# Performance work log

Hardware: AMD Instinct MI355X
Metric: run time of the kernel (lower is better)

## Reference

```python
import jax, jax.numpy as jnp
import numpy as np

N_NODES = 100000
N_EDGES = 3200000
F_IN, F_HID, F_OUT = 128, 16, 32


def setup_inputs() -> dict:
    key = jax.random.key(0)
    k1, k2, k3, k4, k5, k6 = jax.random.split(key, 6)
    x = jax.random.normal(k1, (N_NODES, F_IN), dtype=jnp.float32)
    edge_index = jax.random.randint(k2, (2, N_EDGES), 0, N_NODES, dtype=jnp.int64)
    # Glorot-style init for GCNConv weights, zero bias (PyG defaults)
    W1 = jax.random.normal(k3, (F_IN, F_HID), dtype=jnp.float32) * (1.0 / np.sqrt(F_IN))
    b1 = jnp.zeros((F_HID,), dtype=jnp.float32)
    W2 = jax.random.normal(k4, (F_HID, F_OUT), dtype=jnp.float32) * (1.0 / np.sqrt(F_HID))
    b2 = jnp.zeros((F_OUT,), dtype=jnp.float32)
    return {"x": x, "edge_index": edge_index, "W1": W1, "b1": b1, "W2": W2, "b2": b2}


def reference(x, edge_index, W1, b1, W2, b2):
    N = x.shape[0]
    self_loops = jnp.arange(N, dtype=edge_index.dtype)
    row = jnp.concatenate([edge_index[0], self_loops])  # source nodes
    col = jnp.concatenate([edge_index[1], self_loops])  # target nodes
    # symmetric normalization: deg computed on targets (with self-loops)
    deg = jax.ops.segment_sum(jnp.ones_like(col, dtype=x.dtype), col, num_segments=N)
    dinv = jnp.where(deg > 0, jax.lax.rsqrt(deg), 0.0)
    norm = dinv[row] * dinv[col]  # [E+N]

    def gcn_conv(h, W, b):
        h = h @ W                                   # [N, out]
        msg = h[row] * norm[:, None]                # gather + scale [E+N, out]
        agg = jax.ops.segment_sum(msg, col, num_segments=N)  # scatter-add
        return agg + b

    h = jax.nn.relu(gcn_conv(x, W1, b1))
    # dropout is identity in eval mode
    out = gcn_conv(h, W2, b2)
    return jax.nn.log_softmax(out, axis=1)
```

## Files before the change

### kernel.cpp

```cpp
#include <hip/hip_runtime.h>
#include <math.h>

#define F_IN  128
#define F_HID 16
#define F_OUT 32
#define G     784
#define CSH   9
#define CN    512
#define MAXB  256
#define SCH   4096

typedef unsigned int u32;

__device__ inline float bflo(u32 d) { return __uint_as_float(d << 16); }
__device__ inline float bfhi(u32 d) { return __uint_as_float(d & 0xFFFF0000u); }
__device__ inline u32 f2bf(float f) {
    u32 u = __float_as_uint(f);
    return (u + 0x7FFFu + ((u >> 16) & 1u)) >> 16;
}
__device__ inline u32 pk2(float lo, float hi) { return f2bf(lo) | (f2bf(hi) << 16); }

__global__ void k_hist(const int* __restrict__ col, int E,
                       int* __restrict__ hist_t, int B) {
    __shared__ int h[MAXB];
    int t = threadIdx.x, g = blockIdx.x;
    for (int k = t; k < B; k += 256) h[k] = 0;
    __syncthreads();
    int cg = (E + G - 1) / G;
    int e0 = g * cg, e1 = min(E, e0 + cg);
    for (int e = e0 + t; e < e1; e += 256)
        atomicAdd(&h[col[e] >> CSH], 1);
    __syncthreads();
    for (int b = t; b < B; b += 256) hist_t[(size_t)b * G + g] = h[b];
}

__global__ void k_scan_part(const int* __restrict__ hist_t, int* __restrict__ psum,
                            int M) {
    __shared__ int sd[256];
    int t = threadIdx.x;
    int base = blockIdx.x * SCH + t * 16;
    int s = 0;
#pragma unroll
    for (int k = 0; k < 16; ++k) { int i = base + k; if (i < M) s += hist_t[i]; }
    sd[t] = s;
    __syncthreads();
    for (int o = 128; o > 0; o >>= 1) { if (t < o) sd[t] += sd[t + o]; __syncthreads(); }
    if (t == 0) psum[blockIdx.x] = sd[0];
}

__global__ void k_scan_top(int* __restrict__ psum, int NP) {
    __shared__ int sd[256];
    int t = threadIdx.x;
    int v = (t < NP) ? psum[t] : 0;
    sd[t] = v;
    __syncthreads();
    for (int o = 1; o < 256; o <<= 1) {
        int x = (t >= o) ? sd[t - o] : 0;
        __syncthreads();
        sd[t] += x;
        __syncthreads();
    }
    if (t < NP) psum[t] = sd[t] - v;
}

__global__ void k_scan_out(const int* __restrict__ hist_t, const int* __restrict__ psum,
                           int* __restrict__ off, int M) {
    __shared__ int sd[256];
    int t = threadIdx.x;
    int base = blockIdx.x * SCH + t * 16;
    int v[16], s = 0;
#pragma unroll
    for (int k = 0; k < 16; ++k) {
        v[k] = (base + k < M) ? hist_t[base + k] : 0;
        s += v[k];
    }
    sd[t] = s;
    __syncthreads();
    for (int o = 1; o < 256; o <<= 1) {
        int x = (t >= o) ? sd[t - o] : 0;
        __syncthreads();
        sd[t] += x;
        __syncthreads();
    }
    int run = psum[blockIdx.x] + sd[t] - s;
#pragma unroll
    for (int k = 0; k < 16; ++k) {
        int i = base + k;
        if (i < M) off[i] = run;
        run += v[k];
        if (i == M - 1) off[M] = run;
    }
}

__global__ void k_fill(const int* __restrict__ row, const int* __restrict__ col,
                       int E, const int* __restrict__ off, u32* __restrict__ pairs,
                       int B) {
    __shared__ int cur[MAXB];
    int t = threadIdx.x, g = blockIdx.x;
    for (int b = t; b < B; b += 256) cur[b] = off[(size_t)b * G + g];
    __syncthreads();
    int cg = (E + G - 1) / G;
    int e0 = g * cg, e1 = min(E, e0 + cg);
    for (int e = e0 + t; e < e1; e += 256) {
        int c = col[e];
        int p = atomicAdd(&cur[c >> CSH], 1);
        pairs[p] = ((u32)(c & (CN - 1)) << 17) | (u32)row[e];
    }
}

__global__ void __launch_bounds__(512)
k_sortfine(const u32* __restrict__ pairs, const int* __restrict__ off, int B, int E,
           int* __restrict__ nptr, float* __restrict__ dinv,
           int* __restrict__ srcs, int N) {
    __shared__ int cnt[CN];
    __shared__ int pre[CN];
    int t = threadIdx.x, b = blockIdx.x;
    cnt[t] = 0;
    __syncthreads();
    int s0 = off[(size_t)b * G];
    int s1 = (b == B - 1) ? E : off[(size_t)(b + 1) * G];
    for (int e = s0 + t; e < s1; e += 512)
        atomicAdd(&cnt[pairs[e] >> 17], 1);
    __syncthreads();
    int v = cnt[t];
    pre[t] = v;
    __syncthreads();
    for (int o = 1; o < 512; o <<= 1) {
        int x = (t >= o) ? pre[t - o] : 0;
        __syncthreads();
        pre[t] += x;
        __syncthreads();
    }
    int excl = pre[t] - v;
    int n = (b << CSH) + t;
    nptr[n] = s0 + excl;
    if (b == B - 1 && t == CN - 1) nptr[n + 1] = E;
    if (n < N) dinv[n] = rsqrtf((float)v + 1.0f);
    __syncthreads();
    cnt[t] = s0 + excl;
    __syncthreads();
    for (int e = s0 + t; e < s1; e += 512) {
        u32 p = pairs[e];
        int r = atomicAdd(&cnt[p >> 17], 1);
        srcs[r] = (int)(p & 0x1FFFFu);
    }
}

__global__ void k_gemm1(const float* __restrict__ x, const float* __restrict__ W1,
                        const float* __restrict__ dinv, u32* __restrict__ hs1b, int N) {
    __shared__ float sW[F_IN * F_HID];
    __shared__ float sX[16][F_IN + 4];
    int t = threadIdx.x;
    {
        const float4* W4 = (const float4*)W1;
        float4* sW4 = (float4*)sW;
#pragma unroll
        for (int k = t; k < F_IN * F_HID / 4; k += 256) sW4[k] = W4[k];
    }
    int node0 = blockIdx.x * 16;
    {
        const float4* x4 = (const float4*)(x + (size_t)node0 * F_IN);
#pragma unroll
        for (int k = t; k < 16 * F_IN / 4; k += 256) {
            int r = k >> 5, c4 = k & 31;
            float4 vv = (node0 + r < N) ? x4[k] : make_float4(0.f, 0.f, 0.f, 0.f);
            *(float4*)&sX[r][c4 * 4] = vv;
        }
    }
    __syncthreads();
    int il = t >> 4, j = t & 15;
    float acc = 0.f;
    const float* xr = sX[il];
#pragma unroll 8
    for (int k = 0; k < F_IN; ++k) acc += xr[k] * sW[k * F_HID + j];
    int n = node0 + il;
    float v = (n < N) ? acc * dinv[n] : 0.f;
    float other = __shfl_xor(v, 1);
    if (n < N && !(j & 1)) hs1b[(size_t)n * 8 + (j >> 1)] = pk2(v, other);
}

__device__ inline void gather16(const u32* __restrict__ src, const int* __restrict__ srcs,
                                int e0, int e1, int l, float* a) {
    const uint4* H = (const uint4*)src;
    int e = e0 + l;
    for (; e + 4 < e1; e += 8) {
        int i0 = srcs[e], i1 = srcs[e + 4];
        uint4 d0 = H[(size_t)i0 * 2], d1 = H[(size_t)i0 * 2 + 1];
        uint4 d2 = H[(size_t)i1 * 2], d3 = H[(size_t)i1 * 2 + 1];
        a[0] += bflo(d0.x) + bflo(d2.x);  a[1] += bfhi(d0.x) + bfhi(d2.x);
        a[2] += bflo(d0.y) + bflo(d2.y);  a[3] += bfhi(d0.y) + bfhi(d2.y);
        a[4] += bflo(d0.z) + bflo(d2.z);  a[5] += bfhi(d0.z) + bfhi(d2.z);
        a[6] += bflo(d0.w) + bflo(d2.w);  a[7] += bfhi(d0.w) + bfhi(d2.w);
        a[8] += bflo(d1.x) + bflo(d3.x);  a[9] += bfhi(d1.x) + bfhi(d3.x);
        a[10]+= bflo(d1.y) + bflo(d3.y);  a[11]+= bfhi(d1.y) + bfhi(d3.y);
        a[12]+= bflo(d1.z) + bflo(d3.z);  a[13]+= bfhi(d1.z) + bfhi(d3.z);
        a[14]+= bflo(d1.w) + bflo(d3.w);  a[15]+= bfhi(d1.w) + bfhi(d3.w);
    }
    if (e < e1) {
        int i0 = srcs[e];
        uint4 d0 = H[(size_t)i0 * 2], d1 = H[(size_t)i0 * 2 + 1];
        a[0] += bflo(d0.x);  a[1] += bfhi(d0.x);
        a[2] += bflo(d0.y);  a[3] += bfhi(d0.y);
        a[4] += bflo(d0.z);  a[5] += bfhi(d0.z);
        a[6] += bflo(d0.w);  a[7] += bfhi(d0.w);
        a[8] += bflo(d1.x);  a[9] += bfhi(d1.x);
        a[10]+= bflo(d1.y);  a[11]+= bfhi(d1.y);
        a[12]+= bflo(d1.z);  a[13]+= bfhi(d1.z);
        a[14]+= bflo(d1.w);  a[15]+= bfhi(d1.w);
    }
}

__global__ void k_agg1(const u32* __restrict__ hs1b, const int* __restrict__ srcs,
                       const int* __restrict__ nptr, const float* __restrict__ dinv,
                       const float* __restrict__ b1, u32* __restrict__ h1b, int N) {
    int t = threadIdx.x;
    int g = t >> 2, l = t & 3;
    int n = blockIdx.x * 64 + g;
    if (n >= N) return;
    float a[16];
#pragma unroll
    for (int k = 0; k < 16; ++k) a[k] = 0.f;
    gather16(hs1b, srcs, nptr[n], nptr[n + 1], l, a);
#pragma unroll
    for (int o = 1; o < 4; o <<= 1)
#pragma unroll
        for (int k = 0; k < 16; ++k) a[k] += __shfl_xor(a[k], o, 64);
    uint2 sd = ((const uint2*)hs1b)[(size_t)n * 4 + l];
    float dv = dinv[n];
    float4 bb = ((const float4*)b1)[l];
    float r0 = dv * (a[4 * l]     + bflo(sd.x)) + bb.x;
    float r1 = dv * (a[4 * l + 1] + bfhi(sd.x)) + bb.y;
    float r2 = dv * (a[4 * l + 2] + bflo(sd.y)) + bb.z;
    float r3 = dv * (a[4 * l + 3] + bfhi(sd.y)) + bb.w;
    r0 = fmaxf(r0, 0.f) * dv;  r1 = fmaxf(r1, 0.f) * dv;
    r2 = fmaxf(r2, 0.f) * dv;  r3 = fmaxf(r3, 0.f) * dv;
    ((uint2*)h1b)[(size_t)n * 4 + l] = make_uint2(pk2(r0, r1), pk2(r2, r3));
}

__global__ void k_agg2_final(const u32* __restrict__ h1b, const int* __restrict__ srcs,
                             const int* __restrict__ nptr, const float* __restrict__ dinv,
                             const float* __restrict__ W2, const float* __restrict__ b2,
                             float* __restrict__ out, int N) {
    __shared__ float accS[64 * 17];
    __shared__ float sW2[F_HID * F_OUT];
    __shared__ float sb2[F_OUT];
    int t = threadIdx.x;
    for (int k = t; k < F_HID * F_OUT; k += 256) sW2[k] = W2[k];
    if (t < F_OUT) sb2[t] = b2[t];
    int g = t >> 2, l = t & 3;
    int n = blockIdx.x * 64 + g;
    float a[16];
#pragma unroll
    for (int k = 0; k < 16; ++k) a[k] = 0.f;
    if (n < N) gather16(h1b, srcs, nptr[n], nptr[n + 1], l, a);
#pragma unroll
    for (int o = 1; o < 4; o <<= 1)
#pragma unroll
        for (int k = 0; k < 16; ++k) a[k] += __shfl_xor(a[k], o, 64);
    if (n < N) {
        uint2 sd = ((const uint2*)h1b)[(size_t)n * 4 + l];
        float dv = dinv[n];
        accS[g * 17 + 4 * l]     = dv * (a[4 * l]     + bflo(sd.x));
        accS[g * 17 + 4 * l + 1] = dv * (a[4 * l + 1] + bfhi(sd.x));
        accS[g * 17 + 4 * l + 2] = dv * (a[4 * l + 2] + bflo(sd.y));
        accS[g * 17 + 4 * l + 3] = dv * (a[4 * l + 3] + bfhi(sd.y));
    }
    __syncthreads();
    int g2 = t >> 5, j = t & 31;
    for (int r = 0; r < 8; ++r) {
        int nl = r * 8 + g2;
        int n2 = blockIdx.x * 64 + nl;
        if (n2 < N) {
            float z = sb2[j];
#pragma unroll
            for (int k = 0; k < F_HID; ++k) z += accS[nl * 17 + k] * sW2[k * F_OUT + j];
            float m = z;
            for (int o = 16; o > 0; o >>= 1) m = fmaxf(m, __shfl_xor(m, o, 32));
            float ssum = __expf(z - m);
            for (int o = 16; o > 0; o >>= 1) ssum += __shfl_xor(ssum, o, 32);
            out[(size_t)n2 * F_OUT + j] = z - m - __logf(ssum);
        }
    }
}

static inline size_t alignup(size_t v) { return (v + 255) & ~(size_t)255; }

extern "C" void kernel_launch(void* const* d_in, const int* in_sizes, int n_in,
                              void* d_out, int out_size, void* d_ws, size_t ws_size,
                              hipStream_t stream) {
    const float* x  = (const float*)d_in[0];
    const int*   ei = (const int*)d_in[1];
    const float* W1 = (const float*)d_in[2];
    const float* b1 = (const float*)d_in[3];
    const float* W2 = (const float*)d_in[4];
    const float* b2 = (const float*)d_in[5];
    float* out = (float*)d_out;

    int N = in_sizes[0] / F_IN;
    int E = in_sizes[1] / 2;
    const int* row = ei;
    const int* col = ei + E;
    int B = (N + CN - 1) >> CSH;
    int M = B * G;
    int NP = (M + SCH - 1) / SCH;

    char* w = (char*)d_ws;
    int*   hist_t = (int*)w;   w += alignup(sizeof(int) * (size_t)M);
    int*   off    = (int*)w;   w += alignup(sizeof(int) * ((size_t)M + 1));
    int*   psum   = (int*)w;   w += alignup(sizeof(int) * 256);
    int*   nptr   = (int*)w;   w += alignup(sizeof(int) * ((size_t)B * CN + 1));
    float* dinv   = (float*)w; w += alignup(sizeof(float) * (size_t)N);
    u32*   pairs  = (u32*)w;   w += alignup(sizeof(u32) * (size_t)E);
    int*   srcs   = (int*)w;   w += alignup(sizeof(int) * (size_t)E);
    u32*   hs1b   = (u32*)w;   w += alignup(sizeof(u32) * (size_t)N * 8);
    u32*   h1b    = (u32*)w;

    k_hist<<<G, 256, 0, stream>>>(col, E, hist_t, B);
    k_scan_part<<<NP, 256, 0, stream>>>(hist_t, psum, M);
    k_scan_top<<<1, 256, 0, stream>>>(psum, NP);
    k_scan_out<<<NP, 256, 0, stream>>>(hist_t, psum, off, M);
    k_fill<<<G, 256, 0, stream>>>(row, col, E, off, pairs, B);
    k_sortfine<<<B, 512, 0, stream>>>(pairs, off, B, E, nptr, dinv, srcs, N);

    k_gemm1<<<(N + 15) / 16, 256, 0, stream>>>(x, W1, dinv, hs1b, N);
    k_agg1<<<(N + 63) / 64, 256, 0, stream>>>(hs1b, srcs, nptr, dinv, b1, h1b, N);
    k_agg2_final<<<(N + 63) / 64, 256, 0, stream>>>(h1b, srcs, nptr, dinv, W2, b2, out, N);
}
```

Measured before the change: 260.8 us.

## Shrink sort buckets to 256 nodes and remap blocks across XCDs

Changes the two-level counting sort to use 256-node buckets (CSH 8) with 512 edge groups instead of 784, so the fine-sort kernel runs twice as many 256-thread blocks. It also remaps block indices so consecutive groups and buckets land on the same XCD (p&7 interleave), aiming for L2 locality on the 8-XCD MI355X. The histogram matrix keeps a similar size (B*G) while the fine sort gets more parallelism and smaller shared-memory scans. Bucket count rises to about 391, still under MAXB 512.

```diff
diff --git a/kernel.cpp b/kernel.cpp
--- a/kernel.cpp
+++ b/kernel.cpp
@@ -4,10 +4,10 @@
 #define F_IN  128
 #define F_HID 16
 #define F_OUT 32
-#define G     784
-#define CSH   9
-#define CN    512
-#define MAXB  256
+#define G     512
+#define CSH   8
+#define CN    256
+#define MAXB  512
 #define SCH   4096
 
 typedef unsigned int u32;
@@ -23,7 +23,9 @@
 __global__ void k_hist(const int* __restrict__ col, int E,
                        int* __restrict__ hist_t, int B) {
     __shared__ int h[MAXB];
-    int t = threadIdx.x, g = blockIdx.x;
+    int t = threadIdx.x;
+    int p = blockIdx.x;
+    int g = (p & 7) * (G / 8) + (p >> 3);
     for (int k = t; k < B; k += 256) h[k] = 0;
     __syncthreads();
     int cg = (E + G - 1) / G;
@@ -96,36 +98,41 @@
                        int E, const int* __restrict__ off, u32* __restrict__ pairs,
                        int B) {
     __shared__ int cur[MAXB];
-    int t = threadIdx.x, g = blockIdx.x;
+    int t = threadIdx.x;
+    int p = blockIdx.x;
+    int g = (p & 7) * (G / 8) + (p >> 3);
     for (int b = t; b < B; b += 256) cur[b] = off[(size_t)b * G + g];
     __syncthreads();
     int cg = (E + G - 1) / G;
     int e0 = g * cg, e1 = min(E, e0 + cg);
     for (int e = e0 + t; e < e1; e += 256) {
         int c = col[e];
-        int p = atomicAdd(&cur[c >> CSH], 1);
-        pairs[p] = ((u32)(c & (CN - 1)) << 17) | (u32)row[e];
-    }
-}
-
-__global__ void __launch_bounds__(512)
-k_sortfine(const u32* __restrict__ pairs, const int* __restrict__ off, int B, int E,
-           int* __restrict__ nptr, float* __restrict__ dinv,
-           int* __restrict__ srcs, int N) {
+        int ppos = atomicAdd(&cur[c >> CSH], 1);
+        pairs[ppos] = ((u32)(c & (CN - 1)) << 17) | (u32)row[e];
+    }
+}
+
+__global__ void k_sortfine(const u32* __restrict__ pairs, const int* __restrict__ off,
+                           int B, int chunkB, int E,
+                           int* __restrict__ nptr, float* __restrict__ dinv,
+                           int* __restrict__ srcs, int N) {
     __shared__ int cnt[CN];
     __shared__ int pre[CN];
-    int t = threadIdx.x, b = blockIdx.x;
+    int t = threadIdx.x;
+    int p = blockIdx.x;
+    int b = (p & 7) * chunkB + (p >> 3);
+    if (b >= B) return;
     cnt[t] = 0;
     __syncthreads();
     int s0 = off[(size_t)b * G];
     int s1 = (b == B - 1) ? E : off[(size_t)(b + 1) * G];
-    for (int e = s0 + t; e < s1; e += 512)
+    for (int e = s0 + t; e < s1; e += 256)
         atomicAdd(&cnt[pairs[e] >> 17], 1);
     __syncthreads();
     int v = cnt[t];
     pre[t] = v;
     __syncthreads();
-    for (int o = 1; o < 512; o <<= 1) {
+    for (int o = 1; o < 256; o <<= 1) {
         int x = (t >= o) ? pre[t - o] : 0;
         __syncthreads();
         pre[t] += x;
@@ -139,10 +146,10 @@
     __syncthreads();
     cnt[t] = s0 + excl;
     __syncthreads();
-    for (int e = s0 + t; e < s1; e += 512) {
-        u32 p = pairs[e];
-        int r = atomicAdd(&cnt[p >> 17], 1);
-        srcs[r] = (int)(p & 0x1FFFFu);
+    for (int e = s0 + t; e < s1; e += 256) {
+        u32 pk = pairs[e];
+        int r = atomicAdd(&cnt[pk >> 17], 1);
+        srcs[r] = (int)(pk & 0x1FFFFu);
     }
 }
 
@@ -301,6 +308,7 @@
     const int* row = ei;
     const int* col = ei + E;
     int B = (N + CN - 1) >> CSH;
+    int chunkB = (B + 7) >> 3;
     int M = B * G;
     int NP = (M + SCH - 1) / SCH;
 
@@ -320,7 +328,7 @@
     k_scan_top<<<1, 256, 0, stream>>>(psum, NP);
     k_scan_out<<<NP, 256, 0, stream>>>(hist_t, psum, off, M);
     k_fill<<<G, 256, 0, stream>>>(row, col, E, off, pairs, B);
-    k_sortfine<<<B, 512, 0, stream>>>(pairs, off, B, E, nptr, dinv, srcs, N);
+    k_sortfine<<<chunkB * 8, 256, 0, stream>>>(pairs, off, B, chunkB, E, nptr, dinv, srcs, N);
 
     k_gemm1<<<(N + 15) / 16, 256, 0, stream>>>(x, W1, dinv, hs1b, N);
     k_agg1<<<(N + 63) / 64, 256, 0, stream>>>(hs1b, srcs, nptr, dinv, b1, h1b, N);
```

After: 253.7 us. -2.7%, faster.
